# Performance work log

Measured on AMD Instinct MI355X. Metric: run time of the kernel, lower is better.

The kernel has to match this reference:

```python
import jax, jax.numpy as jnp
import numpy as np
from jax import lax

# shifts generated by _generate_shifts(kernel_size=3): (s1, s2) pairs with
# (s1, s2) >= (0, 0) lexicographically, excluding (0, 0)
SHIFTS = [(0, 1), (1, -1), (1, 0), (1, 1)]


def conv2d_same(x, w, b):
    # x: (B, C_in, H, W), w: (C_out, C_in, kH, kW), b: (C_out,)
    y = lax.conv_general_dilated(
        x, w, window_strides=(1, 1), padding='SAME',
        dimension_numbers=('NCHW', 'OIHW', 'NCHW'))
    return y + b[None, :, None, None]


def setup_inputs() -> dict:
    key = jax.random.key(0)
    k1, k2, k3, k4, k5 = jax.random.split(key, 5)
    B, C_in, C_out, H, W, K = 8, 64, 64, 256, 256, 3
    fan = C_in * K * K
    return {
        'x': jax.random.normal(k1, (B, C_in, H, W), dtype=jnp.float32),
        'w1': jax.random.normal(k2, (C_out, C_in, K, K), dtype=jnp.float32) / np.sqrt(fan),
        'b1': jax.random.normal(k3, (C_out,), dtype=jnp.float32) * 0.01,
        'w2': jax.random.normal(k4, (C_out, C_in, K, K), dtype=jnp.float32) / np.sqrt(fan),
        'b2': jax.random.normal(k5, (C_out,), dtype=jnp.float32) * 0.01,
    }


def reference(x, w1, b1, w2, b2):
    linear_term = conv2d_same(x, w1, b1)
    # torch.roll(x, shifts=(shift_y, shift_x), dims=(2,3)) with
    # circular_shift(x, s1, s2) -> shift_x=s1, shift_y=s2.
    # conv2 is linear, so sum_i conv2(prod_i) == conv2(sum_i prod_i)
    # with the bias added once per shift.
    quad_in = jnp.zeros_like(x)
    for s1, s2 in SHIFTS:
        x_shifted = jnp.roll(x, shift=(s2, s1), axis=(2, 3))
        quad_in = quad_in + jnp.clip(x * x_shifted, -1.0, 1.0)
    quadratic_term = conv2d_same(quad_in, w2, b2 * float(len(SHIFTS)))
    return linear_term + quadratic_term
```

## Files before the change

kernel.cpp:

```cpp
#include <hip/hip_runtime.h>
#include <stdint.h>


typedef short s16x8 __attribute__((ext_vector_type(8)));
typedef float f32x4 __attribute__((ext_vector_type(4)));

__device__ __forceinline__ float clip1(float v) { return fminf(fmaxf(v, -1.f), 1.f); }

__device__ __forceinline__ unsigned short f2bf(float f) {
    union { float f; unsigned u; } v; v.f = f;
    unsigned u = v.u;
    return (unsigned short)((u + 0x7fffu + ((u >> 16) & 1u)) >> 16);
}

__device__ __forceinline__ float bf2f(unsigned short u) {
    union { unsigned v; float f; } t; t.v = ((unsigned)u) << 16; return t.f;
}

__global__ void prep_w(const float* __restrict__ w1, const float* __restrict__ w2,
                       unsigned short* __restrict__ Wb) {
    int idx = blockIdx.x * 256 + threadIdx.x;
    int kk = idx % 96;
    int rest = idx / 96;
    int co = rest & 63; rest >>= 6;
    int cc = rest & 3;
    int kh = rest >> 2;
    int kw = kk >> 5;
    int cci = kk & 31;
    int c2 = cc * 32 + cci;
    const float* src = (c2 < 64) ? w1 : w2;
    int ci = c2 & 63;
    Wb[idx] = f2bf(src[((co * 64 + ci) * 3 + kh) * 3 + kw]);
}

__global__ __launch_bounds__(512, 6) void prep_u4(const float* __restrict__ x,
                                                  unsigned short* __restrict__ U) {
    __shared__ unsigned short X[3][32][270];
    int bid = blockIdx.x;
    int b = bid & 7;
    int rest = bid >> 3;
    int h = rest >> 1;
    int chunk = rest & 1;
    int tid = threadIdx.x;

    for (int it = 0; it < 12; ++it) {
        int idx = tid + (it << 9);
        int w4 = idx & 63;
        int c  = (idx >> 6) & 31;
        int r  = idx >> 11;
        int gr = (h + r + 255) & 255;
        const float4 v = *(const float4*)(x + (((size_t)(b * 64 + chunk * 32 + c)) << 16)
                                            + (gr << 8) + (w4 << 2));
        ushort4 p;
        p.x = f2bf(v.x); p.y = f2bf(v.y); p.z = f2bf(v.z); p.w = f2bf(v.w);
        *(ushort4*)&X[r][c][w4 << 2] = p;
    }
    __syncthreads();

    int c  = tid & 31;
    int ph = (tid >> 5) & 1;
    int wv = tid >> 6;
    int p0 = (wv << 5) + (ph << 4);
    int pm0 = (p0 + 255) & 255;
    float pxc = bf2f(X[1][c][pm0]);
    float pxu = bf2f(X[0][c][pm0]);
    float pxd = bf2f(X[2][c][pm0]);
    size_t base = ((size_t)(((b << 8) + h))) << 8;
    int cx = chunk * 32 + c;
#pragma unroll 4
    for (int i = 0; i < 16; ++i) {
        int p = p0 + i;
        unsigned short xcb = X[1][c][p];
        float xc = bf2f(xcb);
        float xu = bf2f(X[0][c][p]);
        float xd = bf2f(X[2][c][p]);
        float q = clip1(xc * xu) + clip1(xc * pxd) + clip1(xc * pxc) + clip1(xc * pxu);
        size_t po = (base + p) << 7;
        U[po + cx]      = xcb;
        U[po + 64 + cx] = f2bf(q);
        pxc = xc; pxu = xu; pxd = xd;
    }
}

__global__ __launch_bounds__(512, 4) void conv5(
        const unsigned short* __restrict__ U,
        const unsigned short* __restrict__ Wb,
        const float* __restrict__ b1, const float* __restrict__ b2,
        float* __restrict__ out) {
    __shared__ unsigned short Alds[3][64][104];
    __shared__ unsigned short Ib[2][130][40];

    int bid = blockIdx.x;
    int logical = ((bid & 7) << 7) + (bid >> 3);
    int b = logical >> 7;
    int rem = logical & 127;
    int h0 = (rem >> 1) << 2;
    int whalf = rem & 1;
    int w0 = whalf << 7;
    int tid = threadIdx.x;
    int wid = tid >> 6;
    int ln = tid & 63;
    int lr = ln & 15;
    int lq = ln >> 4;
    int rowsel = wid >> 1;
    int pq = wid & 1;
    int o = h0 + rowsel;

    f32x4 acc[4][4];
#pragma unroll
    for (int m = 0; m < 4; m++)
#pragma unroll
        for (int n = 0; n < 4; n++) {
            acc[m][n][0] = 0.f; acc[m][n][1] = 0.f; acc[m][n][2] = 0.f; acc[m][n][3] = 0.f;
        }

    const size_t ubase = ((size_t)b) << 23;

    int cur = 0;
    for (int cc = 0; cc < 4; cc++) {
        for (int i = tid; i < 2304; i += 512) {
            int kh = i / 768;
            int remw = i - kh * 768;
            int co = remw / 12;
            int kk = (remw - co * 12) << 3;
            *(uint4*)&Alds[kh][co][kk] =
                *(const uint4*)&Wb[(((size_t)((kh * 4 + cc) * 64 + co)) * 96) + kk];
        }
        {
            int r = h0 - 1;
            if (r >= 0) {
                const unsigned short* usrc = U + ubase + (((size_t)r) << 15) + cc * 32;
                for (int i = tid; i < 520; i += 512) {
                    int p = i >> 2, q = i & 3;
                    int gcol = w0 + p - 1;
                    uint4 v = (gcol < 0 || gcol > 255) ? make_uint4(0u, 0u, 0u, 0u)
                              : *(const uint4*)&usrc[(((size_t)gcol) << 7) + q * 8];
                    *(uint4*)&Ib[cur][p][q * 8] = v;
                }
            }
        }
        __syncthreads();

        for (int j = 0; j < 6; j++) {
            int rn = h0 + j;
            bool have = (j < 5) && (rn <= 255);
            uint4 s0;
            if (have) {
                const unsigned short* usrc = U + ubase + (((size_t)rn) << 15) + cc * 32;
                int p = tid >> 2, q = tid & 3;
                int gcol = w0 + p - 1;
                s0 = (gcol < 0 || gcol > 255) ? make_uint4(0u, 0u, 0u, 0u)
                     : *(const uint4*)&usrc[(((size_t)gcol) << 7) + q * 8];
            }
            int r = h0 - 1 + j;
            int kh = j - rowsel;
            if (kh >= 0 && kh <= 2 && r >= 0 && r <= 255) {
                __builtin_amdgcn_s_setprio(1);
#pragma unroll
                for (int kw = 0; kw < 3; kw++) {
                    s16x8 af[4], bfr[4];
#pragma unroll
                    for (int m = 0; m < 4; m++)
                        af[m] = *(const s16x8*)&Alds[kh][m * 16 + lr][kw * 32 + lq * 8];
#pragma unroll
                    for (int n = 0; n < 4; n++)
                        bfr[n] = *(const s16x8*)&Ib[cur][(pq << 6) + n * 16 + lr + kw][lq * 8];
#pragma unroll
                    for (int m = 0; m < 4; m++)
#pragma unroll
                        for (int n = 0; n < 4; n++)
                            acc[m][n] = __builtin_amdgcn_mfma_f32_16x16x32_bf16(af[m], bfr[n], acc[m][n], 0, 0, 0);
                }
                __builtin_amdgcn_s_setprio(0);
            }
            if (have) {
                { int p = tid >> 2, q = tid & 3; *(uint4*)&Ib[cur ^ 1][p][q * 8] = s0; }
                if (tid < 8) {
                    int i2 = tid + 512;
                    int p = i2 >> 2, q = i2 & 3;
                    int gcol = w0 + p - 1;
                    const unsigned short* usrc = U + ubase + (((size_t)rn) << 15) + cc * 32;
                    uint4 v = (gcol < 0 || gcol > 255) ? make_uint4(0u, 0u, 0u, 0u)
                              : *(const uint4*)&usrc[(((size_t)gcol) << 7) + q * 8];
                    *(uint4*)&Ib[cur ^ 1][p][q * 8] = v;
                }
            }
            __syncthreads();
            if (j < 5) cur ^= 1;
        }
    }

#pragma unroll
    for (int m = 0; m < 4; m++) {
#pragma unroll
        for (int jj = 0; jj < 4; jj++) {
            int co = m * 16 + lq * 4 + jj;
            float bias = b1[co] + 4.f * b2[co];
#pragma unroll
            for (int n = 0; n < 4; n++) {
                int wpix = w0 + (pq << 6) + n * 16 + lr;
                out[(((size_t)(b * 64 + co)) << 16) + (o << 8) + wpix] = acc[m][n][jj] + bias;
            }
        }
    }
}

__global__ void fallback_conv(const float* __restrict__ x,
                              const float* __restrict__ w1, const float* __restrict__ b1,
                              const float* __restrict__ w2, const float* __restrict__ b2,
                              float* __restrict__ out) {
    size_t idx = (size_t)blockIdx.x * 256 + threadIdx.x;
    int w = idx & 255;
    int h = (int)(idx >> 8) & 255;
    int co = (int)(idx >> 16) & 63;
    int b = (int)(idx >> 22);
    float acc = b1[co] + 4.f * b2[co];
    const float* xb = x + (((size_t)b * 64) << 16);
    for (int ci = 0; ci < 64; ci++) {
        const float* xp = xb + (((size_t)ci) << 16);
        for (int kh = 0; kh < 3; kh++) {
            int hh = h + kh - 1;
            if (hh < 0 || hh > 255) continue;
            for (int kw = 0; kw < 3; kw++) {
                int ww = w + kw - 1;
                if (ww < 0 || ww > 255) continue;
                float xv = xp[(hh << 8) + ww];
                float g1 = w1[((co * 64 + ci) * 3 + kh) * 3 + kw];
                float g2 = w2[((co * 64 + ci) * 3 + kh) * 3 + kw];
                int hm = (hh + 255) & 255, hp = (hh + 1) & 255, wm = (ww + 255) & 255;
                float q = clip1(xv * xp[(hm << 8) + ww]) + clip1(xv * xp[(hp << 8) + wm])
                        + clip1(xv * xp[(hh << 8) + wm]) + clip1(xv * xp[(hm << 8) + wm]);
                acc = fmaf(g1, xv, acc);
                acc = fmaf(g2, q, acc);
            }
        }
    }
    out[idx] = acc;
}

extern "C" void kernel_launch(void* const* d_in, const int* in_sizes, int n_in,
                              void* d_out, int out_size, void* d_ws, size_t ws_size,
                              hipStream_t stream) {
    const float* x  = (const float*)d_in[0];
    const float* w1 = (const float*)d_in[1];
    const float* b1 = (const float*)d_in[2];
    const float* w2 = (const float*)d_in[3];
    const float* b2 = (const float*)d_in[4];
    float* out = (float*)d_out;

    const size_t WB_BYTES = 262144;
    const size_t U_BYTES  = (size_t)8 * 256 * 256 * 128 * 2;
    if (ws_size >= WB_BYTES + U_BYTES) {
        unsigned short* Wb = (unsigned short*)d_ws;
        unsigned short* U  = (unsigned short*)((char*)d_ws + WB_BYTES);
        prep_w<<<dim3(288), dim3(256), 0, stream>>>(w1, w2, Wb);
        prep_u4<<<dim3(4096), dim3(512), 0, stream>>>(x, U);
        conv5<<<dim3(1024), dim3(512), 0, stream>>>(U, Wb, b1, b2, out);
    } else {
        fallback_conv<<<dim3(131072), dim3(256), 0, stream>>>(x, w1, b1, w2, b2, out);
    }
}
```

Before: 163.0 us.

## Retile conv to 8 output rows by 64 columns per block

Changes the per-block output tile from 4 rows by 128 columns to 8 rows by 64 columns. Each of the 8 waves now owns a whole output row instead of half a row, and the input staging buffer shrinks to 66 columns. The goal is to cut the vertical halo overhead: each block now loads 10 input rows for 8 output rows rather than 6 for 4. In exchange the horizontal halo ratio grows, fewer threads take part in each row load, and there are more barrier iterations per channel chunk.

Measured after the change: 188.6 us. +15.7%, slower.

```diff
diff --git a/kernel.cpp b/kernel.cpp
--- a/kernel.cpp
+++ b/kernel.cpp
@@ -82,28 +82,27 @@
     }
 }
 
-__global__ __launch_bounds__(512, 4) void conv5(
+__global__ __launch_bounds__(512, 4) void conv9(
         const unsigned short* __restrict__ U,
         const unsigned short* __restrict__ Wb,
         const float* __restrict__ b1, const float* __restrict__ b2,
         float* __restrict__ out) {
     __shared__ unsigned short Alds[3][64][104];
-    __shared__ unsigned short Ib[2][130][40];
+    __shared__ unsigned short Ib[2][66][40];
 
     int bid = blockIdx.x;
     int logical = ((bid & 7) << 7) + (bid >> 3);
     int b = logical >> 7;
     int rem = logical & 127;
-    int h0 = (rem >> 1) << 2;
-    int whalf = rem & 1;
-    int w0 = whalf << 7;
+    int h0 = (rem >> 2) << 3;
+    int wq = rem & 3;
+    int w0 = wq << 6;
     int tid = threadIdx.x;
     int wid = tid >> 6;
     int ln = tid & 63;
     int lr = ln & 15;
     int lq = ln >> 4;
-    int rowsel = wid >> 1;
-    int pq = wid & 1;
+    int rowsel = wid;
     int o = h0 + rowsel;
 
     f32x4 acc[4][4];
@@ -130,8 +129,8 @@
             int r = h0 - 1;
             if (r >= 0) {
                 const unsigned short* usrc = U + ubase + (((size_t)r) << 15) + cc * 32;
-                for (int i = tid; i < 520; i += 512) {
-                    int p = i >> 2, q = i & 3;
+                if (tid < 264) {
+                    int p = tid >> 2, q = tid & 3;
                     int gcol = w0 + p - 1;
                     uint4 v = (gcol < 0 || gcol > 255) ? make_uint4(0u, 0u, 0u, 0u)
                               : *(const uint4*)&usrc[(((size_t)gcol) << 7) + q * 8];
@@ -141,9 +140,9 @@
         }
         __syncthreads();
 
-        for (int j = 0; j < 6; j++) {
+        for (int j = 0; j < 10; j++) {
             int rn = h0 + j;
-            bool have = (j < 5) && (rn <= 255);
+            bool have = (j < 9) && (rn <= 255) && (tid < 264);
             uint4 s0;
             if (have) {
                 const unsigned short* usrc = U + ubase + (((size_t)rn) << 15) + cc * 32;
@@ -164,7 +163,7 @@
                         af[m] = *(const s16x8*)&Alds[kh][m * 16 + lr][kw * 32 + lq * 8];
 #pragma unroll
                     for (int n = 0; n < 4; n++)
-                        bfr[n] = *(const s16x8*)&Ib[cur][(pq << 6) + n * 16 + lr + kw][lq * 8];
+                        bfr[n] = *(const s16x8*)&Ib[cur][n * 16 + lr + kw][lq * 8];
 #pragma unroll
                     for (int m = 0; m < 4; m++)
 #pragma unroll
@@ -174,19 +173,11 @@
                 __builtin_amdgcn_s_setprio(0);
             }
             if (have) {
-                { int p = tid >> 2, q = tid & 3; *(uint4*)&Ib[cur ^ 1][p][q * 8] = s0; }
-                if (tid < 8) {
-                    int i2 = tid + 512;
-                    int p = i2 >> 2, q = i2 & 3;
-                    int gcol = w0 + p - 1;
-                    const unsigned short* usrc = U + ubase + (((size_t)rn) << 15) + cc * 32;
-                    uint4 v = (gcol < 0 || gcol > 255) ? make_uint4(0u, 0u, 0u, 0u)
-                              : *(const uint4*)&usrc[(((size_t)gcol) << 7) + q * 8];
-                    *(uint4*)&Ib[cur ^ 1][p][q * 8] = v;
-                }
+                int p = tid >> 2, q = tid & 3;
+                *(uint4*)&Ib[cur ^ 1][p][q * 8] = s0;
             }
             __syncthreads();
-            if (j < 5) cur ^= 1;
+            if (j < 9) cur ^= 1;
         }
     }
 
@@ -198,7 +189,7 @@
             float bias = b1[co] + 4.f * b2[co];
 #pragma unroll
             for (int n = 0; n < 4; n++) {
-                int wpix = w0 + (pq << 6) + n * 16 + lr;
+                int wpix = w0 + n * 16 + lr;
                 out[(((size_t)(b * 64 + co)) << 16) + (o << 8) + wpix] = acc[m][n][jj] + bias;
             }
         }
@@ -255,7 +246,7 @@
         unsigned short* U  = (unsigned short*)((char*)d_ws + WB_BYTES);
         prep_w<<<dim3(288), dim3(256), 0, stream>>>(w1, w2, Wb);
         prep_u4<<<dim3(4096), dim3(512), 0, stream>>>(x, U);
-        conv5<<<dim3(1024), dim3(512), 0, stream>>>(U, Wb, b1, b2, out);
+        conv9<<<dim3(1024), dim3(512), 0, stream>>>(U, Wb, b1, b2, out);
     } else {
         fallback_conv<<<dim3(131072), dim3(256), 0, stream>>>(x, w1, b1, w2, b2, out);
     }
```

## Stage two input rows per barrier and prefetch next channel chunk across iterations

Applied to the files above, without the earlier changes.

The conv kernel's row pipeline now loads and double-buffers two input rows per stage, so each channel chunk takes 3 stages and 3 barriers instead of 6. The last stage of each chunk prefetches the first two rows of the next chunk, and the initial rows are loaded once before the loop. This removes the non-overlapped per-chunk halo row load and cuts the barrier count. It doubles the input LDS buffer and raises register pressure from holding two staged rows.

Result: no change. 162.4 us (-0.4%).

```diff
diff --git a/kernel.cpp b/kernel.cpp
--- a/kernel.cpp
+++ b/kernel.cpp
@@ -82,13 +82,13 @@
     }
 }
 
-__global__ __launch_bounds__(512, 4) void conv5(
+__global__ __launch_bounds__(512, 4) void conv10(
         const unsigned short* __restrict__ U,
         const unsigned short* __restrict__ Wb,
         const float* __restrict__ b1, const float* __restrict__ b2,
         float* __restrict__ out) {
     __shared__ unsigned short Alds[3][64][104];
-    __shared__ unsigned short Ib[2][130][40];
+    __shared__ unsigned short Ib[2][2][130][40];
 
     int bid = blockIdx.x;
     int logical = ((bid & 7) << 7) + (bid >> 3);
@@ -115,9 +115,36 @@
         }
 
     const size_t ubase = ((size_t)b) << 23;
+    int sp = tid >> 2, sq = tid & 3;
+    int sgcol = w0 + sp - 1;
+    bool smain_ok = (sgcol >= 0 && sgcol <= 255);
+
+    {
+        for (int rr = 0; rr < 2; ++rr) {
+            int r = h0 - 1 + rr;
+            uint4 v = make_uint4(0u, 0u, 0u, 0u);
+            if (r >= 0 && smain_ok)
+                v = *(const uint4*)(U + ubase + (((size_t)r) << 15)
+                                    + (((size_t)sgcol) << 7) + sq * 8);
+            *(uint4*)&Ib[0][rr][sp][sq * 8] = v;
+        }
+        if (tid < 8) {
+            int i2 = tid + 512;
+            int p = i2 >> 2, q = i2 & 3;
+            int gcol = w0 + p - 1;
+            for (int rr = 0; rr < 2; ++rr) {
+                int r = h0 - 1 + rr;
+                uint4 t = (r < 0 || gcol > 255) ? make_uint4(0u, 0u, 0u, 0u)
+                          : *(const uint4*)(U + ubase + (((size_t)r) << 15)
+                                            + (((size_t)gcol) << 7) + q * 8);
+                *(uint4*)&Ib[0][rr][p][q * 8] = t;
+            }
+        }
+    }
 
     int cur = 0;
     for (int cc = 0; cc < 4; cc++) {
+        int ccoff = cc * 32;
         for (int i = tid; i < 2304; i += 512) {
             int kh = i / 768;
             int remw = i - kh * 768;
@@ -126,67 +153,66 @@
             *(uint4*)&Alds[kh][co][kk] =
                 *(const uint4*)&Wb[(((size_t)((kh * 4 + cc) * 64 + co)) * 96) + kk];
         }
-        {
-            int r = h0 - 1;
-            if (r >= 0) {
-                const unsigned short* usrc = U + ubase + (((size_t)r) << 15) + cc * 32;
-                for (int i = tid; i < 520; i += 512) {
-                    int p = i >> 2, q = i & 3;
-                    int gcol = w0 + p - 1;
-                    uint4 v = (gcol < 0 || gcol > 255) ? make_uint4(0u, 0u, 0u, 0u)
-                              : *(const uint4*)&usrc[(((size_t)gcol) << 7) + q * 8];
-                    *(uint4*)&Ib[cur][p][q * 8] = v;
+        __syncthreads();
+
+        for (int s = 0; s < 3; s++) {
+            int nr0, nr1, noff;
+            bool last = (s == 2);
+            bool havestage = !last || (cc < 3);
+            if (!last) { nr0 = h0 + 1 + 2 * s; nr1 = nr0 + 1; noff = ccoff; }
+            else       { nr0 = h0 - 1;        nr1 = h0;      noff = ccoff + 32; }
+            bool rowA = havestage && nr0 >= 0 && nr0 <= 255;
+            bool rowB = havestage && nr1 >= 0 && nr1 <= 255;
+            uint4 sA = make_uint4(0u, 0u, 0u, 0u), sB = make_uint4(0u, 0u, 0u, 0u);
+            if (rowA && smain_ok)
+                sA = *(const uint4*)(U + ubase + (((size_t)nr0) << 15)
+                                     + (((size_t)sgcol) << 7) + noff + sq * 8);
+            if (rowB && smain_ok)
+                sB = *(const uint4*)(U + ubase + (((size_t)nr1) << 15)
+                                     + (((size_t)sgcol) << 7) + noff + sq * 8);
+            int base2 = 2 * s;
+#pragma unroll
+            for (int kh = 0; kh < 3; kh++) {
+                int t = rowsel + kh;
+                int r = h0 - 1 + t;
+                if (t >= base2 && t <= base2 + 1 && r >= 0 && r <= 255) {
+                    int rr = t - base2;
+                    __builtin_amdgcn_s_setprio(1);
+#pragma unroll
+                    for (int kw = 0; kw < 3; kw++) {
+                        s16x8 af[4], bfr[4];
+#pragma unroll
+                        for (int m = 0; m < 4; m++)
+                            af[m] = *(const s16x8*)&Alds[kh][m * 16 + lr][kw * 32 + lq * 8];
+#pragma unroll
+                        for (int n = 0; n < 4; n++)
+                            bfr[n] = *(const s16x8*)&Ib[cur][rr][(pq << 6) + n * 16 + lr + kw][lq * 8];
+#pragma unroll
+                        for (int m = 0; m < 4; m++)
+#pragma unroll
+                            for (int n = 0; n < 4; n++)
+                                acc[m][n] = __builtin_amdgcn_mfma_f32_16x16x32_bf16(af[m], bfr[n], acc[m][n], 0, 0, 0);
+                    }
+                    __builtin_amdgcn_s_setprio(0);
                 }
             }
-        }
-        __syncthreads();
-
-        for (int j = 0; j < 6; j++) {
-            int rn = h0 + j;
-            bool have = (j < 5) && (rn <= 255);
-            uint4 s0;
-            if (have) {
-                const unsigned short* usrc = U + ubase + (((size_t)rn) << 15) + cc * 32;
-                int p = tid >> 2, q = tid & 3;
+            if (rowA) *(uint4*)&Ib[cur ^ 1][0][sp][sq * 8] = sA;
+            if (rowB) *(uint4*)&Ib[cur ^ 1][1][sp][sq * 8] = sB;
+            if (havestage && tid < 8) {
+                int i2 = tid + 512;
+                int p = i2 >> 2, q = i2 & 3;
                 int gcol = w0 + p - 1;
-                s0 = (gcol < 0 || gcol > 255) ? make_uint4(0u, 0u, 0u, 0u)
-                     : *(const uint4*)&usrc[(((size_t)gcol) << 7) + q * 8];
-            }
-            int r = h0 - 1 + j;
-            int kh = j - rowsel;
-            if (kh >= 0 && kh <= 2 && r >= 0 && r <= 255) {
-                __builtin_amdgcn_s_setprio(1);
-#pragma unroll
-                for (int kw = 0; kw < 3; kw++) {
-                    s16x8 af[4], bfr[4];
-#pragma unroll
-                    for (int m = 0; m < 4; m++)
-                        af[m] = *(const s16x8*)&Alds[kh][m * 16 + lr][kw * 32 + lq * 8];
-#pragma unroll
-                    for (int n = 0; n < 4; n++)
-                        bfr[n] = *(const s16x8*)&Ib[cur][(pq << 6) + n * 16 + lr + kw][lq * 8];
-#pragma unroll
-                    for (int m = 0; m < 4; m++)
-#pragma unroll
-                        for (int n = 0; n < 4; n++)
-                            acc[m][n] = __builtin_amdgcn_mfma_f32_16x16x32_bf16(af[m], bfr[n], acc[m][n], 0, 0, 0);
+                for (int rr = 0; rr < 2; ++rr) {
+                    int r = (rr == 0) ? nr0 : nr1;
+                    if (r < 0 || r > 255) continue;
+                    uint4 t = (gcol > 255) ? make_uint4(0u, 0u, 0u, 0u)
+                              : *(const uint4*)(U + ubase + (((size_t)r) << 15)
+                                                + (((size_t)gcol) << 7) + noff + q * 8);
+                    *(uint4*)&Ib[cur ^ 1][rr][p][q * 8] = t;
                 }
-                __builtin_amdgcn_s_setprio(0);
-            }
-            if (have) {
-                { int p = tid >> 2, q = tid & 3; *(uint4*)&Ib[cur ^ 1][p][q * 8] = s0; }
-                if (tid < 8) {
-                    int i2 = tid + 512;
-                    int p = i2 >> 2, q = i2 & 3;
-                    int gcol = w0 + p - 1;
-                    const unsigned short* usrc = U + ubase + (((size_t)rn) << 15) + cc * 32;
-                    uint4 v = (gcol < 0 || gcol > 255) ? make_uint4(0u, 0u, 0u, 0u)
-                              : *(const uint4*)&usrc[(((size_t)gcol) << 7) + q * 8];
-                    *(uint4*)&Ib[cur ^ 1][p][q * 8] = v;
-                }
             }
             __syncthreads();
-            if (j < 5) cur ^= 1;
+            cur ^= 1;
         }
     }
 
@@ -255,7 +281,7 @@
         unsigned short* U  = (unsigned short*)((char*)d_ws + WB_BYTES);
         prep_w<<<dim3(288), dim3(256), 0, stream>>>(w1, w2, Wb);
         prep_u4<<<dim3(4096), dim3(512), 0, stream>>>(x, U);
-        conv5<<<dim3(1024), dim3(512), 0, stream>>>(U, Wb, b1, b2, out);
+        conv10<<<dim3(1024), dim3(512), 0, stream>>>(U, Wb, b1, b2, out);
     } else {
         fallback_conv<<<dim3(131072), dim3(256), 0, stream>>>(x, w1, b1, w2, b2, out);
     }
```
